# Kernel optimization log

Hardware: AMD Instinct MI355X
Metric: run time of the kernel (lower is better)

The kernel has to match this reference:

```python
import jax, jax.numpy as jnp
import numpy as np

# Config (mirrors HymbaLayer init + env constants)
DIM = 1024; NH = 16; NKV = 4; D = 64          # head_dim = DIM // NH
NATTN = NH // 2; NSSM = NH // 2; KVREP = NATTN // NKV
S = 16          # _HYMBA_SSM_STATE
NMETA = 4       # _HYMBA_META_TOK
BASE = 10000.0  # rope_base
CHUNK = 64      # _HYMBA_SCAN_CHUNK
B, T = 2, 2048


def _rms_norm(x, eps=1e-6):
    return x * jax.lax.rsqrt(jnp.mean(x * x, -1, keepdims=True) + eps)


def _rotary_cs(t_len, d, base):
    inv = 1.0 / (base ** (jnp.arange(0, d, 2, dtype=jnp.float32) / d))  # (d/2,)
    f = jnp.arange(t_len, dtype=jnp.float32)[:, None] * inv[None, :]    # (T, d/2)
    return jnp.cos(f), jnp.sin(f)


def _apply_rot(x, cos, sin):
    # x: (B, H, T, D); rotate-half style rotary
    d2 = x.shape[-1] // 2
    x1, x2 = x[..., :d2], x[..., d2:]
    c, s = cos[None, None], sin[None, None]
    return jnp.concatenate([x1 * c - x2 * s, x1 * s + x2 * c], -1)


def _scan_chunks(log_a, u, chunk):
    # Exact chunk-parallel diagonal scan: h_t = exp(log_a_t)*h_{t-1} + u_t
    b, t, s = u.shape
    nc = t // chunk
    la = log_a.reshape(b, nc, chunk, s)
    uu = u.reshape(b, nc, chunk, s)
    log_p = jnp.clip(jnp.cumsum(la, axis=2), -30.0, 0.0)
    p = jnp.exp(log_p)
    h_local = p * jnp.cumsum(uu * jnp.exp(-log_p), axis=2)

    def step(h0, args):
        hl, pc = args                          # (B, chunk, S)
        hc = hl + pc * h0[:, None, :]
        return hc[:, -1], hc

    _, hs = jax.lax.scan(step, jnp.zeros((b, s), u.dtype),
                         (jnp.swapaxes(h_local, 0, 1), jnp.swapaxes(p, 0, 1)))
    return jnp.swapaxes(hs, 0, 1).reshape(b, t, s)


def _mamba_head(logA, Bw, Cw, dtw, dtb, Ow, x):
    # x: (B, T, D); selective SSM with diagonal A
    dt = jnp.minimum(jax.nn.softplus(x @ dtw.T + dtb), 1.0)   # (B,T,S)
    A = jnp.minimum(-jnp.exp(logA), 10.0)                      # (S,)
    log_a = jnp.clip(dt * A, -0.5, 0.0)
    Bx = (x @ Bw.T) * dt
    Cc = x @ Cw.T
    h = _scan_chunks(log_a, Bx, CHUNK)                         # (B,T,S)
    y = jnp.sum(Cc * h, -1, keepdims=True)
    return h @ Ow.T + y * x[..., :1]


def _forward(x, meta_tokens, c_q_w, c_k_w, c_v_w, q_gain, ssm_in_w, proj_w,
             attn_scale, ssm_scale, ssm_logA, ssm_Bw, ssm_Cw, ssm_dtw, ssm_dtb, ssm_Ow):
    b, t, c = x.shape
    x_ext = jnp.concatenate([jnp.broadcast_to(meta_tokens, (b, NMETA, c)), x], 1)
    t_ext = t + NMETA
    q = (x_ext @ c_q_w.T).reshape(b, t_ext, NH, D).transpose(0, 2, 1, 3)
    k = (x_ext @ c_k_w.T).reshape(b, t_ext, NKV, D).transpose(0, 2, 1, 3)
    v = (x_ext @ c_v_w.T).reshape(b, t_ext, NKV, D).transpose(0, 2, 1, 3)
    q = _rms_norm(q); k = _rms_norm(k)
    cos, sin = _rotary_cs(t_ext, D, BASE)
    q = _apply_rot(q, cos, sin); k = _apply_rot(k, cos, sin)
    # GQA attention over the first NATTN heads, causal over T_ext
    q_attn = q[:, :NATTN] * q_gain[None, :, None, None]
    k_exp = jnp.repeat(k, KVREP, axis=1)
    v_exp = jnp.repeat(v, KVREP, axis=1)
    scores = jnp.einsum('bhqd,bhkd->bhqk', q_attn, k_exp) / jnp.sqrt(jnp.float32(D))
    mask = jnp.tril(jnp.ones((t_ext, t_ext), bool))
    scores = jnp.where(mask[None, None], scores, -jnp.inf)
    attn = jax.nn.softmax(scores, axis=-1)
    ao = jnp.einsum('bhqk,bhkd->bhqd', attn, v_exp)
    ao = ao[:, :, NMETA:].transpose(0, 2, 1, 3).reshape(b, t, NATTN * D) * attn_scale
    # SSM branch on the original (un-prepended) tokens
    ssm_x = (x @ ssm_in_w.T).reshape(b, t, NSSM, D)
    ssm_out = jax.vmap(_mamba_head, in_axes=(0, 0, 0, 0, 0, 0, 2), out_axes=2)(
        ssm_logA, ssm_Bw, ssm_Cw, ssm_dtw, ssm_dtb, ssm_Ow, ssm_x)
    ssm_out = ssm_out.reshape(b, t, NSSM * D) * ssm_scale
    return jnp.concatenate([ao, ssm_out], -1) @ proj_w.T


def setup_inputs() -> dict:
    key = jax.random.key(0)
    ks = jax.random.split(key, 16)
    r = lambda k, sh, sc=0.02: jax.random.normal(k, sh, jnp.float32) * sc
    return {
        'x': jax.random.normal(ks[0], (B, T, DIM), jnp.float32),
        'meta_tokens': r(ks[1], (1, NMETA, DIM)),
        'c_q_w': r(ks[2], (DIM, DIM)),
        'c_k_w': r(ks[3], (NKV * D, DIM)),
        'c_v_w': r(ks[4], (NKV * D, DIM)),
        'q_gain': jnp.full((NATTN,), 1.0, jnp.float32),
        'ssm_in_w': r(ks[5], (NSSM * D, DIM)),
        'proj_w': r(ks[6], (DIM, DIM)),
        'attn_scale': jnp.ones((1,), jnp.float32),
        'ssm_scale': jnp.ones((1,), jnp.float32),
        'ssm_logA': jax.random.normal(ks[7], (NSSM, S), jnp.float32) * 0.5,
        'ssm_Bw': r(ks[8], (NSSM, S, D), 0.05),
        'ssm_Cw': r(ks[9], (NSSM, S, D), 0.05),
        'ssm_dtw': r(ks[10], (NSSM, S, D), 0.05),
        'ssm_dtb': jnp.full((NSSM, S), -4.0, jnp.float32),
        'ssm_Ow': r(ks[11], (NSSM, D, S), 0.05),
    }


def reference(x, meta_tokens, c_q_w, c_k_w, c_v_w, q_gain, ssm_in_w, proj_w,
              attn_scale, ssm_scale, ssm_logA, ssm_Bw, ssm_Cw, ssm_dtw, ssm_dtb, ssm_Ow):
    return _forward(x, meta_tokens, c_q_w, c_k_w, c_v_w, q_gain, ssm_in_w, proj_w,
                    attn_scale, ssm_scale, ssm_logA, ssm_Bw, ssm_Cw, ssm_dtw, ssm_dtb, ssm_Ow)
```

## Files before the change

kernel.cpp:

```cpp
#include <hip/hip_runtime.h>
#include <hip/hip_bf16.h>
#include <math.h>

typedef __hip_bfloat16 bf16;
typedef __attribute__((ext_vector_type(8))) short short8;
typedef __attribute__((ext_vector_type(4))) float f32x4;

static constexpr int kB = 2;
static constexpr int kT = 2048;
static constexpr int kDIM = 1024;
static constexpr int kNMETA = 4;
static constexpr int kTEXT = kT + kNMETA;
static constexpr int kMEXT = kB * kTEXT;
static constexpr int kMPAD = 4224;
static constexpr int kMX = kB * kT;
static constexpr int kQT = 33;
static constexpr int kTP = 2112;

static constexpr size_t oXE = 0;
static constexpr size_t oYB = 0;
static constexpr size_t oLU = 8650752;
static constexpr size_t oCC = oLU + (size_t)kMX * 128 * 8;
static constexpr size_t oHL = oCC + (size_t)kMX * 128 * 4;
static constexpr size_t oX0 = oHL + (size_t)kMX * 128 * 2;
static constexpr size_t oQP = oX0 + (size_t)kMX * 8 * 4;
static constexpr size_t oKP = oQP + (size_t)kB * 8 * kTP * 64 * 2;
static constexpr size_t oVT = oKP + (size_t)kB * 4 * kTP * 64 * 2;
static constexpr size_t oWP = oVT + (size_t)kB * 4 * 64 * kTP * 2;
static constexpr size_t oWQ = oWP + (size_t)1024 * 1024 * 2;
static constexpr size_t oAO = 134217728;
static constexpr size_t oAL = oAO + (size_t)2 * kB * 8 * kTP * 64 * 4;

#define GLD_LDS16(gp, lp)                                                          \
  __builtin_amdgcn_global_load_lds((const __attribute__((address_space(1))) void*)(gp), \
                                   (__attribute__((address_space(3))) void*)(lp), 16, 0, 0)

__device__ __forceinline__ short bf2s(float f) {
  union { bf16 h; short s; } u;
  u.h = __float2bfloat16(f);
  return u.s;
}

__device__ __forceinline__ uint4 pack8(float4 a, float4 b) {
  union { bf16 h[8]; uint4 v; } u;
  u.h[0] = __float2bfloat16(a.x); u.h[1] = __float2bfloat16(a.y);
  u.h[2] = __float2bfloat16(a.z); u.h[3] = __float2bfloat16(a.w);
  u.h[4] = __float2bfloat16(b.x); u.h[5] = __float2bfloat16(b.y);
  u.h[6] = __float2bfloat16(b.z); u.h[7] = __float2bfloat16(b.w);
  return u.v;
}

__global__ __launch_bounds__(256) void prep_all(const float* __restrict__ cq, const float* __restrict__ ck,
                                                const float* __restrict__ cv, const float* __restrict__ sw,
                                                const float* __restrict__ pw,
                                                const float* __restrict__ x, const float* __restrict__ meta,
                                                bf16* __restrict__ wqkvsx, bf16* __restrict__ wproj,
                                                bf16* __restrict__ xe,
                                                bf16* __restrict__ Qp, bf16* __restrict__ Kp,
                                                bf16* __restrict__ Vt) {
  int i = blockIdx.x * 256 + threadIdx.x;
  if (i < 327680) {
    int row = i >> 7, v = i & 127;
    const float* src; bf16* dst;
    if (row < 512)       { src = cq + (size_t)row * 1024;          dst = wqkvsx + (size_t)row * 1024; }
    else if (row < 768)  { src = ck + (size_t)(row - 512) * 1024;  dst = wqkvsx + (size_t)row * 1024; }
    else if (row < 1024) { src = cv + (size_t)(row - 768) * 1024;  dst = wqkvsx + (size_t)row * 1024; }
    else if (row < 1536) { src = sw + (size_t)(row - 1024) * 1024; dst = wqkvsx + (size_t)row * 1024; }
    else                 { src = pw + (size_t)(row - 1536) * 1024; dst = wproj + (size_t)(row - 1536) * 1024; }
    float4 a0 = ((const float4*)src)[v * 2], a1 = ((const float4*)src)[v * 2 + 1];
    ((uint4*)dst)[v] = pack8(a0, a1);
  } else if (i < 868352) {
    int j = i - 327680;
    int r = j >> 7, v = j & 127;
    uint4 val = {0u, 0u, 0u, 0u};
    if (r < kMEXT) {
      int b = r / kTEXT, te = r - b * kTEXT;
      const float* src = (te < kNMETA) ? (meta + (size_t)te * kDIM)
                                       : (x + ((size_t)b * kT + (te - kNMETA)) * kDIM);
      float4 a0 = ((const float4*)src)[v * 2];
      float4 a1 = ((const float4*)src)[v * 2 + 1];
      val = pack8(a0, a1);
    }
    ((uint4*)(xe + (size_t)r * kDIM))[v] = val;
  } else {
    int j = i - 868352;
    if (j < 30720) {
      int k = j & 31, te = (j >> 5) % 60, bh = j / (60 * 32);
      *(unsigned int*)(Qp + ((size_t)bh * kTP + 2052 + te) * 64 + k * 2) = 0u;
    } else if (j < 46080) {
      int jj = j - 30720;
      int k = jj & 31, te = (jj >> 5) % 60, bh = jj / (60 * 32);
      *(unsigned int*)(Kp + ((size_t)bh * kTP + 2052 + te) * 64 + k * 2) = 0u;
    } else if (j < 61440) {
      int jj = j - 46080;
      int k = jj % 30, rowd = jj / 30;
      *(unsigned int*)(Vt + (size_t)rowd * kTP + 2052 + k * 2) = 0u;
    }
  }
}

template <int MODE>
__global__ __launch_bounds__(256) void gemm_t(const bf16* __restrict__ A,
                                              const bf16* __restrict__ W,
                                              void* __restrict__ O0, void* __restrict__ O1,
                                              void* __restrict__ O2,
                                              const float* __restrict__ q_gain,
                                              const float* __restrict__ dtw, const float* __restrict__ dtb,
                                              const float* __restrict__ Bw, const float* __restrict__ Cw,
                                              const float* __restrict__ logA,
                                              float* __restrict__ LU, float* __restrict__ CC,
                                              float* __restrict__ X0) {
  constexpr int SMEM_SZ = (MODE == 0) ? 25344 : 12288;
  __shared__ char smem[SMEM_SZ];
  const int tid = threadIdx.x;
  const int wave = tid >> 6, lane = tid & 63;
  const int quad = lane >> 4, l16 = lane & 15;
  const int bm = blockIdx.y * 128, bn = blockIdx.x * 64;
  const int srow = tid >> 2, scol = (tid & 3) * 8;
  const bf16* ag0 = A + (size_t)(bm + srow) * 1024 + scol;
  const bf16* ag1 = A + (size_t)(bm + 64 + srow) * 1024 + scol;
  const bf16* bg0 = W + (size_t)(bn + srow) * 1024 + scol;
  char* asb = smem + wave * 1024;
  char* bsb = smem + 8192 + wave * 1024;
  f32x4 acc[2][4] = {};
  for (int k0 = 0; k0 < 1024; k0 += 32) {
    __syncthreads();
    GLD_LDS16(ag0, asb);
    GLD_LDS16(ag1, asb + 4096);
    GLD_LDS16(bg0, bsb);
    ag0 += 32; ag1 += 32; bg0 += 32;
    __syncthreads();
    short8 af[2], bfr[4];
#pragma unroll
    for (int mi = 0; mi < 2; ++mi)
      af[mi] = *(const short8*)(smem + (size_t)(wave * 32 + mi * 16 + l16) * 64 + quad * 16);
#pragma unroll
    for (int ni = 0; ni < 4; ++ni)
      bfr[ni] = *(const short8*)(smem + 8192 + (size_t)(ni * 16 + l16) * 64 + quad * 16);
#pragma unroll
    for (int mi = 0; mi < 2; ++mi)
#pragma unroll
      for (int ni = 0; ni < 4; ++ni)
        acc[mi][ni] = __builtin_amdgcn_mfma_f32_16x16x32_bf16(af[mi], bfr[ni], acc[mi][ni], 0, 0, 0);
  }
  if constexpr (MODE == 2) {
#pragma unroll
    for (int mi = 0; mi < 2; ++mi)
#pragma unroll
      for (int ni = 0; ni < 4; ++ni) {
        int colg = bn + ni * 16 + l16;
#pragma unroll
        for (int r = 0; r < 4; ++r) {
          int row = bm + wave * 32 + mi * 16 + quad * 4 + r;
          ((float*)O0)[(size_t)row * 1024 + colg] = acc[mi][ni][r];
        }
      }
  } else {
    const int tile = blockIdx.x;
    if (tile < 16) {
      float gain = (tile < 8) ? q_gain[tile] * 0.125f : 1.f;
      float inv0 = exp2f(-13.287712379549449f * (float)l16 * (1.f / 32.f));
      float inv1 = exp2f(-13.287712379549449f * (float)(l16 + 16) * (1.f / 32.f));
#pragma unroll
      for (int mi = 0; mi < 2; ++mi) {
        int row0 = bm + wave * 32 + mi * 16 + quad * 4;
        if (row0 >= kMEXT) continue;
        int b = row0 >= kTEXT ? 1 : 0;
        int te0 = row0 - b * kTEXT;
        if (tile < 12) {
          float ss[4];
#pragma unroll
          for (int r = 0; r < 4; ++r) {
            float s = 0.f;
#pragma unroll
            for (int ni = 0; ni < 4; ++ni) s += acc[mi][ni][r] * acc[mi][ni][r];
#pragma unroll
            for (int off = 1; off < 16; off <<= 1) s += __shfl_xor(s, off, 64);
            ss[r] = s;
          }
          bf16* base = (tile < 8)
            ? (bf16*)O0 + (((size_t)(b * 8 + tile)) * kTP + te0) * 64 + l16
            : (bf16*)O1 + (((size_t)(b * 4 + tile - 8)) * kTP + te0) * 64 + l16;
#pragma unroll
          for (int r = 0; r < 4; ++r) {
            float rn = rsqrtf(ss[r] * (1.f / 64.f) + 1e-6f) * gain;
            float te = (float)(te0 + r);
            float a0 = te * inv0, a1 = te * inv1;
            float c0 = __cosf(a0), s0 = __sinf(a0);
            float c1 = __cosf(a1), s1 = __sinf(a1);
            float v0 = acc[mi][0][r] * rn, v1 = acc[mi][1][r] * rn;
            float v2 = acc[mi][2][r] * rn, v3 = acc[mi][3][r] * rn;
            bf16* dst = base + (size_t)r * 64;
            dst[0]  = __float2bfloat16(v0 * c0 - v2 * s0);
            dst[16] = __float2bfloat16(v1 * c1 - v3 * s1);
            dst[32] = __float2bfloat16(v0 * s0 + v2 * c0);
            dst[48] = __float2bfloat16(v1 * s1 + v3 * c1);
          }
        } else {
          int hv = tile - 12;
#pragma unroll
          for (int ni = 0; ni < 4; ++ni) {
            union { unsigned long long q; bf16 hh[4]; } pw;
#pragma unroll
            for (int r = 0; r < 4; ++r) pw.hh[r] = __float2bfloat16(acc[mi][ni][r]);
            *(unsigned long long*)((bf16*)O2 +
                (((size_t)(b * 4 + hv)) * 64 + ni * 16 + l16) * kTP + te0) = pw.q;
          }
        }
      }
    } else {
      const int hd = tile - 16;
      __syncthreads();
      short (*Xl)[72] = (short(*)[72])smem;
      short (*Wl)[72] = (short(*)[72])(smem + 18432);
#pragma unroll
      for (int mi = 0; mi < 2; ++mi) {
        if (l16 == 0) {
#pragma unroll
          for (int r = 0; r < 4; ++r) {
            int row = bm + wave * 32 + mi * 16 + quad * 4 + r;
            if (row < kMEXT) {
              int bb = row >= kTEXT ? 1 : 0;
              int te = row - bb * kTEXT;
              if (te >= kNMETA) X0[(size_t)(bb * kT + te - kNMETA) * 8 + hd] = acc[mi][0][r];
            }
          }
        }
      }
#pragma unroll
      for (int mi = 0; mi < 2; ++mi)
#pragma unroll
        for (int ni = 0; ni < 4; ++ni)
#pragma unroll
          for (int r = 0; r < 4; ++r)
            Xl[wave * 32 + mi * 16 + quad * 4 + r][ni * 16 + l16] = bf2s(acc[mi][ni][r]);
      for (int s2 = tid; s2 < 384; s2 += 256) {
        int row = s2 >> 3, v = s2 & 7;
        const float* src = (row < 16) ? dtw + ((size_t)(hd * 16 + row)) * 64
                         : (row < 32) ? Bw + ((size_t)(hd * 16 + row - 16)) * 64
                                      : Cw + ((size_t)(hd * 16 + row - 32)) * 64;
        float4 a0 = ((const float4*)src)[v * 2];
        float4 a1 = ((const float4*)src)[v * 2 + 1];
        *(uint4*)&Wl[row][v * 8] = pack8(a0, a1);
      }
      __syncthreads();
      f32x4 a3[2][3] = {};
#pragma unroll
      for (int mt = 0; mt < 2; ++mt) {
        short8 xa0 = *(const short8*)&Xl[wave * 32 + mt * 16 + l16][quad * 8];
        short8 xa1 = *(const short8*)&Xl[wave * 32 + mt * 16 + l16][32 + quad * 8];
#pragma unroll
        for (int nb = 0; nb < 3; ++nb) {
          short8 wb0 = *(const short8*)&Wl[nb * 16 + l16][quad * 8];
          a3[mt][nb] = __builtin_amdgcn_mfma_f32_16x16x32_bf16(xa0, wb0, a3[mt][nb], 0, 0, 0);
          short8 wb1 = *(const short8*)&Wl[nb * 16 + l16][32 + quad * 8];
          a3[mt][nb] = __builtin_amdgcn_mfma_f32_16x16x32_bf16(xa1, wb1, a3[mt][nb], 0, 0, 0);
        }
      }
      float dtb_v = dtb[hd * 16 + l16];
      float A_v = fminf(-expf(logA[hd * 16 + l16]), 10.f);
#pragma unroll
      for (int mt = 0; mt < 2; ++mt)
#pragma unroll
        for (int r = 0; r < 4; ++r) {
          int row = bm + wave * 32 + mt * 16 + quad * 4 + r;
          if (row >= kMEXT) continue;
          int bb = row >= kTEXT ? 1 : 0;
          int te = row - bb * kTEXT;
          if (te < kNMETA) continue;
          size_t ix = (size_t)(bb * kT + te - kNMETA) * 128 + hd * 16 + l16;
          float raw = a3[mt][0][r] + dtb_v;
          float sp = fmaxf(raw, 0.f) + log1pf(expf(-fabsf(raw)));
          float dt = fminf(sp, 1.f);
          float lav = fminf(fmaxf(dt * A_v, -0.5f), 0.f);
          *(float2*)(LU + 2 * ix) = make_float2(lav, a3[mt][1][r] * dt);
          CC[ix] = a3[mt][2][r];
        }
    }
  }
}

__global__ __launch_bounds__(256) void attn_part(const bf16* __restrict__ Qp,
                                                 const bf16* __restrict__ Kp,
                                                 const bf16* __restrict__ Vt,
                                                 float* __restrict__ AO, float* __restrict__ AL) {
  __shared__ short Ks[64][72];
  __shared__ short Vs[64][72];
  __shared__ short Ps[4][16][72];
  const int part = blockIdx.x & 1;
  const int qt = (kQT - 1) - (blockIdx.x >> 1);
  const int h = blockIdx.y, b = blockIdx.z;
  const int kvh = h >> 1;
  const int tid = threadIdx.x, wave = tid >> 6, lane = tid & 63;
  const int quad = lane >> 4, l16 = lane & 15;
  const int hsplit = (qt + 2) >> 1;
  const int kt_begin = part == 0 ? 0 : hsplit;
  const int kt_end = part == 0 ? hsplit : qt + 1;

  short8 qf[2];
  {
    const bf16* qrow = Qp + (((size_t)(b * 8 + h)) * kTP + qt * 64 + wave * 16 + l16) * 64 + quad * 8;
    qf[0] = *(const short8*)(qrow);
    qf[1] = *(const short8*)(qrow + 32);
  }
  short8 ones;
#pragma unroll
  for (int i = 0; i < 8; ++i) ones[i] = (short)0x3F80;

  const bf16* kbase = Kp + ((size_t)(b * 4 + kvh)) * kTP * 64;
  const bf16* vbase = Vt + ((size_t)(b * 4 + kvh)) * 64 * kTP;

  const int r0row = tid >> 3, r0c8 = tid & 7;
  const int r1row = (256 + tid) >> 3, r1c8 = tid & 7;

  f32x4 O[4] = {};
  f32x4 lacc = {};
  const int q_abs = qt * 64 + wave * 16 + l16;

  uint4 kr0 = *(const uint4*)(kbase + (size_t)(kt_begin * 64 + r0row) * 64 + r0c8 * 8);
  uint4 kr1 = *(const uint4*)(kbase + (size_t)(kt_begin * 64 + r1row) * 64 + r1c8 * 8);
  uint4 vr0 = *(const uint4*)(vbase + (size_t)r0row * kTP + kt_begin * 64 + r0c8 * 8);
  uint4 vr1 = *(const uint4*)(vbase + (size_t)r1row * kTP + kt_begin * 64 + r1c8 * 8);

  for (int kt = kt_begin; kt < kt_end; ++kt) {
    __syncthreads();
    *(uint4*)&Ks[r0row][r0c8 * 8] = kr0;
    *(uint4*)&Ks[r1row][r1c8 * 8] = kr1;
    *(uint4*)&Vs[r0row][r0c8 * 8] = vr0;
    *(uint4*)&Vs[r1row][r1c8 * 8] = vr1;
    if (kt + 1 < kt_end) {
      int kn = (kt + 1) * 64;
      kr0 = *(const uint4*)(kbase + (size_t)(kn + r0row) * 64 + r0c8 * 8);
      kr1 = *(const uint4*)(kbase + (size_t)(kn + r1row) * 64 + r1c8 * 8);
      vr0 = *(const uint4*)(vbase + (size_t)r0row * kTP + kn + r0c8 * 8);
      vr1 = *(const uint4*)(vbase + (size_t)r1row * kTP + kn + r1c8 * 8);
    }
    __syncthreads();

    f32x4 st[4] = {};
#pragma unroll
    for (int nb = 0; nb < 4; ++nb) {
      short8 ak0 = *(const short8*)&Ks[nb * 16 + l16][quad * 8];
      st[nb] = __builtin_amdgcn_mfma_f32_16x16x32_bf16(ak0, qf[0], st[nb], 0, 0, 0);
      short8 ak1 = *(const short8*)&Ks[nb * 16 + l16][32 + quad * 8];
      st[nb] = __builtin_amdgcn_mfma_f32_16x16x32_bf16(ak1, qf[1], st[nb], 0, 0, 0);
    }
    if (kt == qt) {
      int key0 = kt * 64 + quad * 4;
#pragma unroll
      for (int nb = 0; nb < 4; ++nb)
#pragma unroll
        for (int rg = 0; rg < 4; ++rg)
          if (key0 + nb * 16 + rg > q_abs) st[nb][rg] = -1e30f;
    }
#pragma unroll
    for (int nb = 0; nb < 4; ++nb) {
      union { unsigned long long q; bf16 hh[4]; } pw;
#pragma unroll
      for (int rg = 0; rg < 4; ++rg) pw.hh[rg] = __float2bfloat16(__expf(st[nb][rg]));
      *(unsigned long long*)&Ps[wave][l16][nb * 16 + quad * 4] = pw.q;
    }
    short8 pf0 = *(const short8*)&Ps[wave][l16][quad * 8];
    short8 pf1 = *(const short8*)&Ps[wave][l16][32 + quad * 8];
    lacc = __builtin_amdgcn_mfma_f32_16x16x32_bf16(pf0, ones, lacc, 0, 0, 0);
    lacc = __builtin_amdgcn_mfma_f32_16x16x32_bf16(pf1, ones, lacc, 0, 0, 0);
#pragma unroll
    for (int db = 0; db < 4; ++db) {
      short8 bv0 = *(const short8*)&Vs[db * 16 + l16][quad * 8];
      O[db] = __builtin_amdgcn_mfma_f32_16x16x32_bf16(pf0, bv0, O[db], 0, 0, 0);
      short8 bv1 = *(const short8*)&Vs[db * 16 + l16][32 + quad * 8];
      O[db] = __builtin_amdgcn_mfma_f32_16x16x32_bf16(pf1, bv1, O[db], 0, 0, 0);
    }
  }
  size_t hb = (((size_t)part * 2 + b) * 8 + h);
  float* aoB = AO + hb * kTP * 64;
  float* alB = AL + hb * kTP;
#pragma unroll
  for (int rg = 0; rg < 4; ++rg) {
    int q = qt * 64 + wave * 16 + quad * 4 + rg;
    float* dst = aoB + (size_t)q * 64 + l16;
#pragma unroll
    for (int db = 0; db < 4; ++db) dst[db * 16] = O[db][rg];
    if (l16 == 0) alB[q] = lacc[rg];
  }
}

__global__ __launch_bounds__(256) void ssm_scan(const float* __restrict__ LU, bf16* __restrict__ HL) {
  __shared__ float sH[4][64], sP[4][64], sH0[4][64];
  const int tid = threadIdx.x;
  const int ch = tid & 3, c = tid >> 2;
  const int chain = blockIdx.x * 4 + ch;
  const int b = chain >> 7, hs = chain & 127;
  const float2* LU2 = (const float2*)LU;
  const size_t base = ((size_t)b * kT) * 128 + hs;
  float H = 0.f, cum = 0.f;
  for (int i = 0; i < 32; ++i) {
    float2 lu = LU2[base + (size_t)(c * 32 + i) * 128];
    cum += lu.x;
    H = __expf(lu.x) * H + lu.y;
  }
  sH[ch][c] = H;
  sP[ch][c] = __expf(cum);
  __syncthreads();
  const int wv = tid >> 6, lane = tid & 63;
  float Hs = sH[wv][lane], Ps = sP[wv][lane];
#pragma unroll
  for (int off = 1; off < 64; off <<= 1) {
    float Hp = __shfl_up(Hs, off, 64);
    float Pp = __shfl_up(Ps, off, 64);
    if (lane >= off) { Hs = Hs + Ps * Hp; Ps = Ps * Pp; }
  }
  float Hex = __shfl_up(Hs, 1, 64);
  if (lane == 0) Hex = 0.f;
  sH0[wv][lane] = Hex;
  __syncthreads();
  float h = sH0[ch][c];
  for (int i = 0; i < 32; ++i) {
    size_t ix = base + (size_t)(c * 32 + i) * 128;
    float2 lu = LU2[ix];
    h = __expf(lu.x) * h + lu.y;
    HL[ix] = __float2bfloat16(h);
  }
}

__global__ __launch_bounds__(256) void combine_out(const float* __restrict__ AO,
                                                   const float* __restrict__ AL,
                                                   const float* __restrict__ attn_scale,
                                                   const bf16* __restrict__ HL, const float* __restrict__ CC,
                                                   const float* __restrict__ X0, const float* __restrict__ Ow,
                                                   const float* __restrict__ ssm_scale,
                                                   bf16* __restrict__ Y) {
  if (blockIdx.x < 528) {
    int id = blockIdx.x * 256 + threadIdx.x;
    int d16 = id & 3;
    int tmp = id >> 2;
    int q = tmp % kTP; tmp /= kTP;
    int h = tmp & 7, b = tmp >> 3;
    if (q < kNMETA || q >= kTEXT) return;
    size_t hb0 = ((size_t)b * 8 + h), hb1 = ((size_t)(2 + b) * 8 + h);
    float l = AL[hb0 * kTP + q] + AL[hb1 * kTP + q];
    float so = attn_scale[0] / fmaxf(l, 1e-30f);
    const float4* p0 = (const float4*)(AO + (hb0 * kTP + q) * 64 + d16 * 16);
    const float4* p1 = (const float4*)(AO + (hb1 * kTP + q) * 64 + d16 * 16);
    bf16* dst = Y + ((size_t)(b * kT + q - kNMETA)) * kDIM + h * 64 + d16 * 16;
#pragma unroll
    for (int i = 0; i < 4; ++i) {
      float4 a = p0[i], c = p1[i];
      dst[i * 4 + 0] = __float2bfloat16((a.x + c.x) * so);
      dst[i * 4 + 1] = __float2bfloat16((a.y + c.y) * so);
      dst[i * 4 + 2] = __float2bfloat16((a.z + c.z) * so);
      dst[i * 4 + 3] = __float2bfloat16((a.w + c.w) * so);
    }
  } else {
    int id = (blockIdx.x - 528) * 256 + threadIdx.x;
    int d4 = id & 3, h = (id >> 2) & 7, t = (id >> 5) & 2047, b = id >> 16;
    size_t ix0 = ((size_t)(b * kT + t)) * 128 + h * 16;
    float hv[16], y = 0.f;
#pragma unroll
    for (int s = 0; s < 16; ++s) {
      float v = __bfloat162float(HL[ix0 + s]);
      hv[s] = v;
      y += CC[ix0 + s] * v;
    }
    float x0 = X0[(size_t)(b * kT + t) * 8 + h];
    float scl = ssm_scale[0];
    const float* ow = Ow + ((size_t)h * 64 + d4 * 16) * 16;
    bf16* dst = Y + ((size_t)(b * kT + t)) * kDIM + 512 + h * 64 + d4 * 16;
    float yx = y * x0;
#pragma unroll
    for (int d = 0; d < 16; ++d) {
      float acc = yx;
      const float* owr = ow + d * 16;
#pragma unroll
      for (int s = 0; s < 16; ++s) acc += hv[s] * owr[s];
      dst[d] = __float2bfloat16(acc * scl);
    }
  }
}

extern "C" void kernel_launch(void* const* d_in, const int* in_sizes, int n_in,
                              void* d_out, int out_size, void* d_ws, size_t ws_size,
                              hipStream_t stream) {
  (void)in_sizes; (void)n_in; (void)out_size; (void)ws_size;
  const float* x        = (const float*)d_in[0];
  const float* meta     = (const float*)d_in[1];
  const float* c_q_w    = (const float*)d_in[2];
  const float* c_k_w    = (const float*)d_in[3];
  const float* c_v_w    = (const float*)d_in[4];
  const float* q_gain   = (const float*)d_in[5];
  const float* ssm_in_w = (const float*)d_in[6];
  const float* proj_w   = (const float*)d_in[7];
  const float* attn_sc  = (const float*)d_in[8];
  const float* ssm_sc   = (const float*)d_in[9];
  const float* ssm_logA = (const float*)d_in[10];
  const float* ssm_Bw   = (const float*)d_in[11];
  const float* ssm_Cw   = (const float*)d_in[12];
  const float* ssm_dtw  = (const float*)d_in[13];
  const float* ssm_dtb  = (const float*)d_in[14];
  const float* ssm_Ow   = (const float*)d_in[15];

  char* w = (char*)d_ws;
  bf16*  XE = (bf16*)(w + oXE);
  bf16*  YB = (bf16*)(w + oYB);
  bf16*  QP = (bf16*)(w + oQP);
  bf16*  KP = (bf16*)(w + oKP);
  bf16*  VT = (bf16*)(w + oVT);
  bf16*  WQ = (bf16*)(w + oWQ);
  bf16*  WP = (bf16*)(w + oWP);
  float* LU = (float*)(w + oLU);
  float* CC = (float*)(w + oCC);
  bf16*  HL = (bf16*)(w + oHL);
  float* X0 = (float*)(w + oX0);
  float* AO = (float*)(w + oAO);
  float* AL = (float*)(w + oAL);

  prep_all<<<3632, 256, 0, stream>>>(c_q_w, c_k_w, c_v_w, ssm_in_w, proj_w,
                                     x, meta, WQ, WP, XE, QP, KP, VT);

  gemm_t<0><<<dim3(24, kMPAD / 128), 256, 0, stream>>>(XE, WQ, QP, KP, VT, q_gain,
                                                       ssm_dtw, ssm_dtb, ssm_Bw, ssm_Cw,
                                                       ssm_logA, LU, CC, X0);

  attn_part<<<dim3(kQT * 2, 8, kB), 256, 0, stream>>>(QP, KP, VT, AO, AL);

  ssm_scan<<<64, 256, 0, stream>>>(LU, HL);

  combine_out<<<1040, 256, 0, stream>>>(AO, AL, attn_sc, HL, CC, X0, ssm_Ow, ssm_sc, YB);

  gemm_t<2><<<dim3(16, kMX / 128), 256, 0, stream>>>(YB, WP, d_out, nullptr, nullptr, nullptr,
                                                     nullptr, nullptr, nullptr, nullptr, nullptr,
                                                     nullptr, nullptr, nullptr);
}
```

Measured before the change: 226.9 us.

## Split attention KV range three ways and double the GEMM K-step

New measurement: 213.8 us. -5.8%, faster.

```diff
diff --git a/kernel.cpp b/kernel.cpp
--- a/kernel.cpp
+++ b/kernel.cpp
@@ -29,7 +29,7 @@
 static constexpr size_t oWP = oVT + (size_t)kB * 4 * 64 * kTP * 2;
 static constexpr size_t oWQ = oWP + (size_t)1024 * 1024 * 2;
 static constexpr size_t oAO = 134217728;
-static constexpr size_t oAL = oAO + (size_t)2 * kB * 8 * kTP * 64 * 4;
+static constexpr size_t oAL = oAO + (size_t)3 * kB * 8 * kTP * 64 * 4;
 
 #define GLD_LDS16(gp, lp)                                                          \
   __builtin_amdgcn_global_load_lds((const __attribute__((address_space(1))) void*)(gp), \
@@ -110,38 +110,49 @@
                                               const float* __restrict__ logA,
                                               float* __restrict__ LU, float* __restrict__ CC,
                                               float* __restrict__ X0) {
-  constexpr int SMEM_SZ = (MODE == 0) ? 25344 : 12288;
+  constexpr int SMEM_SZ = (MODE == 0) ? 25344 : 24576;
   __shared__ char smem[SMEM_SZ];
   const int tid = threadIdx.x;
   const int wave = tid >> 6, lane = tid & 63;
   const int quad = lane >> 4, l16 = lane & 15;
   const int bm = blockIdx.y * 128, bn = blockIdx.x * 64;
-  const int srow = tid >> 2, scol = (tid & 3) * 8;
-  const bf16* ag0 = A + (size_t)(bm + srow) * 1024 + scol;
-  const bf16* ag1 = A + (size_t)(bm + 64 + srow) * 1024 + scol;
-  const bf16* bg0 = W + (size_t)(bn + srow) * 1024 + scol;
-  char* asb = smem + wave * 1024;
-  char* bsb = smem + 8192 + wave * 1024;
+  const bf16* ag0 = A + (size_t)(bm + (tid >> 2)) * 1024 + (tid & 3) * 8;
+  const bf16* ag1 = A + (size_t)(bm + 64 + (tid >> 2)) * 1024 + (tid & 3) * 8;
+  const bf16* bg0 = W + (size_t)(bn + (tid >> 2)) * 1024 + (tid & 3) * 8;
+  char* a00 = smem + wave * 1024;
+  char* a10 = smem + 4096 + wave * 1024;
+  char* a01 = smem + 8192 + wave * 1024;
+  char* a11 = smem + 12288 + wave * 1024;
+  char* bs0 = smem + 16384 + wave * 1024;
+  char* bs1 = smem + 20480 + wave * 1024;
   f32x4 acc[2][4] = {};
-  for (int k0 = 0; k0 < 1024; k0 += 32) {
+  for (int k0 = 0; k0 < 1024; k0 += 64) {
     __syncthreads();
-    GLD_LDS16(ag0, asb);
-    GLD_LDS16(ag1, asb + 4096);
-    GLD_LDS16(bg0, bsb);
-    ag0 += 32; ag1 += 32; bg0 += 32;
+    GLD_LDS16(ag0, a00);
+    GLD_LDS16(ag0 + 32, a01);
+    GLD_LDS16(ag1, a10);
+    GLD_LDS16(ag1 + 32, a11);
+    GLD_LDS16(bg0, bs0);
+    GLD_LDS16(bg0 + 32, bs1);
+    ag0 += 64; ag1 += 64; bg0 += 64;
     __syncthreads();
-    short8 af[2], bfr[4];
-#pragma unroll
-    for (int mi = 0; mi < 2; ++mi)
-      af[mi] = *(const short8*)(smem + (size_t)(wave * 32 + mi * 16 + l16) * 64 + quad * 16);
-#pragma unroll
-    for (int ni = 0; ni < 4; ++ni)
-      bfr[ni] = *(const short8*)(smem + 8192 + (size_t)(ni * 16 + l16) * 64 + quad * 16);
-#pragma unroll
-    for (int mi = 0; mi < 2; ++mi)
+#pragma unroll
+    for (int p = 0; p < 2; ++p) {
+      short8 af[2], bfr[4];
+#pragma unroll
+      for (int mi = 0; mi < 2; ++mi)
+        af[mi] = *(const short8*)(smem + p * 8192 +
+                                  (size_t)(wave * 32 + mi * 16 + l16) * 64 + quad * 16);
 #pragma unroll
       for (int ni = 0; ni < 4; ++ni)
-        acc[mi][ni] = __builtin_amdgcn_mfma_f32_16x16x32_bf16(af[mi], bfr[ni], acc[mi][ni], 0, 0, 0);
+        bfr[ni] = *(const short8*)(smem + 16384 + p * 4096 +
+                                   (size_t)(ni * 16 + l16) * 64 + quad * 16);
+#pragma unroll
+      for (int mi = 0; mi < 2; ++mi)
+#pragma unroll
+        for (int ni = 0; ni < 4; ++ni)
+          acc[mi][ni] = __builtin_amdgcn_mfma_f32_16x16x32_bf16(af[mi], bfr[ni], acc[mi][ni], 0, 0, 0);
+    }
   }
   if constexpr (MODE == 2) {
 #pragma unroll
@@ -287,15 +298,17 @@
   __shared__ short Ks[64][72];
   __shared__ short Vs[64][72];
   __shared__ short Ps[4][16][72];
-  const int part = blockIdx.x & 1;
-  const int qt = (kQT - 1) - (blockIdx.x >> 1);
+  const int part = blockIdx.x % 3;
+  const int qt = (kQT - 1) - (blockIdx.x / 3);
   const int h = blockIdx.y, b = blockIdx.z;
   const int kvh = h >> 1;
   const int tid = threadIdx.x, wave = tid >> 6, lane = tid & 63;
   const int quad = lane >> 4, l16 = lane & 15;
-  const int hsplit = (qt + 2) >> 1;
-  const int kt_begin = part == 0 ? 0 : hsplit;
-  const int kt_end = part == 0 ? hsplit : qt + 1;
+  const int ntiles = qt + 1;
+  const int s1 = ntiles / 3, s2 = (2 * ntiles) / 3;
+  const int kt_begin = (part == 0) ? 0 : (part == 1 ? s1 : s2);
+  const int kt_end = (part == 0) ? s1 : (part == 1 ? s2 : ntiles);
+  const int kt_pf = (kt_begin < kt_end) ? kt_begin : 0;
 
   short8 qf[2];
   {
@@ -317,10 +330,10 @@
   f32x4 lacc = {};
   const int q_abs = qt * 64 + wave * 16 + l16;
 
-  uint4 kr0 = *(const uint4*)(kbase + (size_t)(kt_begin * 64 + r0row) * 64 + r0c8 * 8);
-  uint4 kr1 = *(const uint4*)(kbase + (size_t)(kt_begin * 64 + r1row) * 64 + r1c8 * 8);
-  uint4 vr0 = *(const uint4*)(vbase + (size_t)r0row * kTP + kt_begin * 64 + r0c8 * 8);
-  uint4 vr1 = *(const uint4*)(vbase + (size_t)r1row * kTP + kt_begin * 64 + r1c8 * 8);
+  uint4 kr0 = *(const uint4*)(kbase + (size_t)(kt_pf * 64 + r0row) * 64 + r0c8 * 8);
+  uint4 kr1 = *(const uint4*)(kbase + (size_t)(kt_pf * 64 + r1row) * 64 + r1c8 * 8);
+  uint4 vr0 = *(const uint4*)(vbase + (size_t)r0row * kTP + kt_pf * 64 + r0c8 * 8);
+  uint4 vr1 = *(const uint4*)(vbase + (size_t)r1row * kTP + kt_pf * 64 + r1c8 * 8);
 
   for (int kt = kt_begin; kt < kt_end; ++kt) {
     __syncthreads();
@@ -437,19 +450,20 @@
     int q = tmp % kTP; tmp /= kTP;
     int h = tmp & 7, b = tmp >> 3;
     if (q < kNMETA || q >= kTEXT) return;
-    size_t hb0 = ((size_t)b * 8 + h), hb1 = ((size_t)(2 + b) * 8 + h);
-    float l = AL[hb0 * kTP + q] + AL[hb1 * kTP + q];
+    size_t hb0 = ((size_t)b * 8 + h), hb1 = ((size_t)(2 + b) * 8 + h), hb2 = ((size_t)(4 + b) * 8 + h);
+    float l = AL[hb0 * kTP + q] + AL[hb1 * kTP + q] + AL[hb2 * kTP + q];
     float so = attn_scale[0] / fmaxf(l, 1e-30f);
     const float4* p0 = (const float4*)(AO + (hb0 * kTP + q) * 64 + d16 * 16);
     const float4* p1 = (const float4*)(AO + (hb1 * kTP + q) * 64 + d16 * 16);
+    const float4* p2 = (const float4*)(AO + (hb2 * kTP + q) * 64 + d16 * 16);
     bf16* dst = Y + ((size_t)(b * kT + q - kNMETA)) * kDIM + h * 64 + d16 * 16;
 #pragma unroll
     for (int i = 0; i < 4; ++i) {
-      float4 a = p0[i], c = p1[i];
-      dst[i * 4 + 0] = __float2bfloat16((a.x + c.x) * so);
-      dst[i * 4 + 1] = __float2bfloat16((a.y + c.y) * so);
-      dst[i * 4 + 2] = __float2bfloat16((a.z + c.z) * so);
-      dst[i * 4 + 3] = __float2bfloat16((a.w + c.w) * so);
+      float4 a = p0[i], c = p1[i], e = p2[i];
+      dst[i * 4 + 0] = __float2bfloat16((a.x + c.x + e.x) * so);
+      dst[i * 4 + 1] = __float2bfloat16((a.y + c.y + e.y) * so);
+      dst[i * 4 + 2] = __float2bfloat16((a.z + c.z + e.z) * so);
+      dst[i * 4 + 3] = __float2bfloat16((a.w + c.w + e.w) * so);
     }
   } else {
     int id = (blockIdx.x - 528) * 256 + threadIdx.x;
@@ -521,7 +535,7 @@
                                                        ssm_dtw, ssm_dtb, ssm_Bw, ssm_Cw,
                                                        ssm_logA, LU, CC, X0);
 
-  attn_part<<<dim3(kQT * 2, 8, kB), 256, 0, stream>>>(QP, KP, VT, AO, AL);
+  attn_part<<<dim3(kQT * 3, 8, kB), 256, 0, stream>>>(QP, KP, VT, AO, AL);
 
   ssm_scan<<<64, 256, 0, stream>>>(LU, HL);
 
```
